# Kernel optimization log

Hardware: AMD Instinct MI355X
Metric: run time of the kernel (lower is better)

The kernel has to match this reference:

```python
import jax, jax.numpy as jnp
import numpy as np

N_HEADS = 8
KEY_DIM = 64
MEM_DIM = 64
HEAD_DIM = 64
IN_DIM = 256
OUT_DIM = 256


def setup_inputs() -> dict:
    key = jax.random.key(0)
    ks = jax.random.split(key, 7)
    x = jax.random.normal(ks[0], (8, IN_DIM, 64, 64), dtype=jnp.float32)
    # learned params
    key_p = jax.random.uniform(ks[1], (N_HEADS, KEY_DIM, MEM_DIM), dtype=jnp.float32)
    memory = jax.random.uniform(ks[2], (N_HEADS, MEM_DIM, HEAD_DIM), dtype=jnp.float32) * 0.5 - 0.25
    w_in = jax.random.normal(ks[3], (N_HEADS * KEY_DIM, IN_DIM), dtype=jnp.float32) * (1.0 / np.sqrt(IN_DIM))
    b_in = jax.random.normal(ks[4], (N_HEADS * KEY_DIM,), dtype=jnp.float32) * 0.01
    w_out = jax.random.normal(ks[5], (OUT_DIM, N_HEADS * HEAD_DIM), dtype=jnp.float32) * (1.0 / np.sqrt(N_HEADS * HEAD_DIM))
    b_out = jax.random.normal(ks[6], (OUT_DIM,), dtype=jnp.float32) * 0.01
    return {"x": x, "key_p": key_p, "memory": memory, "w_in": w_in, "b_in": b_in, "w_out": w_out, "b_out": b_out}


def reference(x, key_p, memory, w_in, b_in, w_out, b_out):
    B, _, H, W = x.shape
    # 1x1 conv projection: [B, n_heads*key_dim, H, W]
    out = jnp.einsum('oc,bchw->bohw', w_in, x) + b_in[None, :, None, None]
    # split heads: b (k n) h w -> b n k h w  (einops '(c m)' with m=n_heads => c is outer)
    out = out.reshape(B, KEY_DIM, N_HEADS, H, W).transpose(0, 2, 1, 3, 4)
    # per-head key matmul over key_dim -> memory_dim
    out = jnp.einsum('nkm,bnkhw->bnmhw', key_p, out)
    out = jax.nn.softmax(out, axis=2)
    # per-head memory matmul over memory_dim -> head_dim
    out = jnp.einsum('nmd,bnmhw->bndhw', memory, out)
    # merge heads: b n d h w -> b (d n) h w  (einops 'b m c h w -> b (m c) h w' with m=heads... wait)
    # einops 'b m c h w -> b (m c) h w': m (heads) is outer -> transpose then reshape
    out = out.reshape(B, N_HEADS * HEAD_DIM, H, W)
    # final 1x1 conv
    out = jnp.einsum('oc,bchw->bohw', w_out, out) + b_out[None, :, None, None]
    return out
```

## Files before the change

kernel.cpp:

```cpp
#include <hip/hip_runtime.h>


typedef _Float16 half8 __attribute__((ext_vector_type(8)));
typedef _Float16 half4 __attribute__((ext_vector_type(4)));
typedef _Float16 half2v __attribute__((ext_vector_type(2)));
typedef float float4v __attribute__((ext_vector_type(4)));

__device__ _Float16 g_Aswz[512 * 256];
__device__ _Float16 g_Mswz[256 * 512];
__device__ float    g_bb[512];

__global__ __launch_bounds__(256) void fold_all(
    const float* __restrict__ key_p, const float* __restrict__ w_in,
    const float* __restrict__ b_in, const float* __restrict__ w_out,
    const float* __restrict__ memory)
{
    __shared__ float sv[512];
    const int blk = blockIdx.x;
    const int t = threadIdx.x;

    if (blk < 512) {
        const int row = blk, n = row >> 6, m = row & 63;
        if (t < 64) sv[t] = key_p[n * 4096 + t * 64 + m];
        __syncthreads();
        const int c = t;
        float v = 0.f;
        #pragma unroll 8
        for (int k = 0; k < 64; ++k)
            v = fmaf(sv[k], w_in[(k * 8 + n) * 256 + c], v);
        int R = row >> 4, s = c >> 5, i = c & 7;
        int lidx = (row & 15) + 16 * ((c >> 3) & 3);
        g_Aswz[(((R * 8 + s) * 64 + lidx) << 3) + i] = (_Float16)v;
        if (t < 64) {
            float r2 = sv[t] * b_in[t * 8 + n];
            r2 += __shfl_down(r2, 32, 64);
            r2 += __shfl_down(r2, 16, 64);
            r2 += __shfl_down(r2, 8, 64);
            r2 += __shfl_down(r2, 4, 64);
            r2 += __shfl_down(r2, 2, 64);
            r2 += __shfl_down(r2, 1, 64);
            if (t == 0) g_bb[row] = r2;
        }
    } else {
        const int o = blk - 512;
        sv[t]       = w_out[o * 512 + t];
        sv[256 + t] = w_out[o * 512 + 256 + t];
        __syncthreads();
        #pragma unroll
        for (int hh = 0; hh < 2; ++hh) {
            int col = t + hh * 256, n = col >> 6, m = col & 63;
            const float4* mrow = (const float4*)(memory + n * 4096 + m * 64);
            const float4* wrow = (const float4*)(sv + n * 64);
            float v = 0.f;
            #pragma unroll
            for (int qd = 0; qd < 16; ++qd) {
                float4 a = mrow[qd], wv = wrow[qd];
                v += a.x * wv.x + a.y * wv.y + a.z * wv.z + a.w * wv.w;
            }
            int R2 = o >> 4, s = col >> 5, i = col & 7;
            int lidx = (o & 15) + 16 * ((col >> 3) & 3);
            g_Mswz[(((R2 * 16 + s) * 64 + lidx) << 3) + i] = (_Float16)v;
        }
    }
}

#define XS_STRIDE 264

__global__ __launch_bounds__(512) void fused_main(
    const float* __restrict__ x, const float* __restrict__ b_out,
    float* __restrict__ out)
{
    __shared__ _Float16 S[32768];

    const int t  = threadIdx.x;
    const int w  = t >> 6;
    const int l  = t & 63;
    const int q  = l >> 4;
    const int lp = l & 15;
    const int wg  = blockIdx.x;
    const int b   = wg >> 6;
    const int hw0 = (wg & 63) * 64;
    const float* xb = x + (size_t)b * 256 * 4096 + hw0;

    {
        const int m_ = t & 15;
        const int tc = t >> 4;
        #pragma unroll
        for (int i = 0; i < 4; ++i) {
            const int cp = i * 32 + tc;
            const int c0 = cp * 2;
            const float* p0 = xb + (size_t)c0 * 4096 + m_;
            const float* p1 = p0 + 4096;
            float a0 = p0[0],  a1 = p0[16], a2 = p0[32], a3 = p0[48];
            float b0 = p1[0],  b1 = p1[16], b2 = p1[32], b3 = p1[48];
            *(half2v*)(&S[(m_ +  0) * XS_STRIDE + c0]) = half2v{(_Float16)a0, (_Float16)b0};
            *(half2v*)(&S[(m_ + 16) * XS_STRIDE + c0]) = half2v{(_Float16)a1, (_Float16)b1};
            *(half2v*)(&S[(m_ + 32) * XS_STRIDE + c0]) = half2v{(_Float16)a2, (_Float16)b2};
            *(half2v*)(&S[(m_ + 48) * XS_STRIDE + c0]) = half2v{(_Float16)a3, (_Float16)b3};
        }
    }
    __syncthreads();

    float4v acc[4][4];
    #pragma unroll
    for (int r = 0; r < 4; ++r)
        #pragma unroll
        for (int c = 0; c < 4; ++c) acc[r][c] = float4v{0.f, 0.f, 0.f, 0.f};

    const half8* Ag = (const half8*)g_Aswz;
    for (int s = 0; s < 8; ++s) {
        half8 bf[4];
        #pragma unroll
        for (int c = 0; c < 4; ++c)
            bf[c] = *(const half8*)(&S[(c * 16 + lp) * XS_STRIDE + s * 32 + q * 8]);
        half8 af[4];
        #pragma unroll
        for (int r = 0; r < 4; ++r)
            af[r] = Ag[((w * 4 + r) * 8 + s) * 64 + l];
        #pragma unroll
        for (int r = 0; r < 4; ++r)
            #pragma unroll
            for (int c = 0; c < 4; ++c)
                acc[r][c] = __builtin_amdgcn_mfma_f32_16x16x32_f16(af[r], bf[c], acc[r][c], 0, 0, 0);
    }

    #pragma unroll
    for (int r = 0; r < 4; ++r) {
        float4v bbv = *(const float4v*)(g_bb + w * 64 + r * 16 + q * 4);
        #pragma unroll
        for (int c = 0; c < 4; ++c)
            #pragma unroll
            for (int j = 0; j < 4; ++j) acc[r][c][j] += bbv[j];
    }

    __syncthreads();

    #pragma unroll
    for (int c = 0; c < 4; ++c) {
        float mx = -1e30f;
        #pragma unroll
        for (int r = 0; r < 4; ++r)
            #pragma unroll
            for (int j = 0; j < 4; ++j) mx = fmaxf(mx, acc[r][c][j]);
        mx = fmaxf(mx, __shfl_xor(mx, 16, 64));
        mx = fmaxf(mx, __shfl_xor(mx, 32, 64));
        float sum = 0.f;
        #pragma unroll
        for (int r = 0; r < 4; ++r)
            #pragma unroll
            for (int j = 0; j < 4; ++j) {
                float e = __expf(acc[r][c][j] - mx);
                acc[r][c][j] = e;
                sum += e;
            }
        sum += __shfl_xor(sum, 16, 64);
        sum += __shfl_xor(sum, 32, 64);
        float inv = 1.f / sum;
        #pragma unroll
        for (int r = 0; r < 4; ++r) {
            int s2 = w * 2 + (r >> 1);
            int lq = ((r & 1) * 2 + (q >> 1)) * 16 + lp;
            int i0 = (q & 1) * 4;
            half4 pv = {(_Float16)(acc[r][c][0] * inv), (_Float16)(acc[r][c][1] * inv),
                        (_Float16)(acc[r][c][2] * inv), (_Float16)(acc[r][c][3] * inv)};
            *(half4*)(&S[(((s2 * 4 + c) * 64) + lq) * 8 + i0]) = pv;
        }
    }
    __syncthreads();

    float4v acc2[2][4];
    #pragma unroll
    for (int r = 0; r < 2; ++r)
        #pragma unroll
        for (int c = 0; c < 4; ++c) acc2[r][c] = float4v{0.f, 0.f, 0.f, 0.f};

    const half8* Mg = (const half8*)g_Mswz;
    for (int s2 = 0; s2 < 16; ++s2) {
        half8 bf2[4];
        #pragma unroll
        for (int c = 0; c < 4; ++c)
            bf2[c] = *(const half8*)(&S[(((s2 * 4 + c) * 64) + l) * 8]);
        half8 af2[2];
        #pragma unroll
        for (int r = 0; r < 2; ++r)
            af2[r] = Mg[((w * 2 + r) * 16 + s2) * 64 + l];
        #pragma unroll
        for (int r = 0; r < 2; ++r)
            #pragma unroll
            for (int c = 0; c < 4; ++c)
                acc2[r][c] = __builtin_amdgcn_mfma_f32_16x16x32_f16(af2[r], bf2[c], acc2[r][c], 0, 0, 0);
    }

    #pragma unroll
    for (int r = 0; r < 2; ++r) {
        int ob = w * 32 + r * 16 + q * 4;
        float4v bo = *(const float4v*)(b_out + ob);
        #pragma unroll
        for (int j = 0; j < 4; ++j) {
            float* orow = out + ((size_t)b * 256 + ob + j) * 4096 + hw0;
            #pragma unroll
            for (int c = 0; c < 4; ++c)
                orow[c * 16 + lp] = acc2[r][c][j] + bo[j];
        }
    }
}

extern "C" void kernel_launch(void* const* d_in, const int* in_sizes, int n_in,
                              void* d_out, int out_size, void* d_ws, size_t ws_size,
                              hipStream_t stream) {
    (void)in_sizes; (void)n_in; (void)ws_size; (void)out_size; (void)d_ws;
    const float* x      = (const float*)d_in[0];
    const float* key_p  = (const float*)d_in[1];
    const float* memory = (const float*)d_in[2];
    const float* w_in   = (const float*)d_in[3];
    const float* b_in   = (const float*)d_in[4];
    const float* w_out  = (const float*)d_in[5];
    const float* b_out  = (const float*)d_in[6];
    float* out = (float*)d_out;

    fold_all<<<768, 256, 0, stream>>>(key_p, w_in, b_in, w_out, memory);
    fused_main<<<512, 512, 0, stream>>>(x, b_out, out);
}
```

Measured before the change: 117.5 us.

## Process two pixel tiles per workgroup, prefetching the second tile into registers

Each workgroup now handles two 64-pixel tiles instead of one and launches 256 workgroups instead of 512. The second tile's x values are loaded into registers during the first tile's GEMM and then written to a separate LDS region, so the global load latency overlaps with compute. LDS grows to about 130KB and the softmax output gets its own region, which removes one barrier. The costs are fewer workgroups (256 on a GPU with 256 CUs, so one per CU), more register pressure, and no longer overlapping across workgroups.

```diff
diff --git a/kernel.cpp b/kernel.cpp
--- a/kernel.cpp
+++ b/kernel.cpp
@@ -65,38 +65,56 @@
 }
 
 #define XS_STRIDE 264
+#define XS1 16896
+#define PB  33792
 
 __global__ __launch_bounds__(512) void fused_main(
     const float* __restrict__ x, const float* __restrict__ b_out,
     float* __restrict__ out)
 {
-    __shared__ _Float16 S[32768];
+    __shared__ _Float16 S[66560];
 
     const int t  = threadIdx.x;
     const int w  = t >> 6;
     const int l  = t & 63;
     const int q  = l >> 4;
     const int lp = l & 15;
-    const int wg  = blockIdx.x;
-    const int b   = wg >> 6;
-    const int hw0 = (wg & 63) * 64;
-    const float* xb = x + (size_t)b * 256 * 4096 + hw0;
+    const int wg = blockIdx.x;
+    const int tile0 = wg * 2, tile1 = wg * 2 + 1;
+    const int b0 = tile0 >> 6, hw00 = (tile0 & 63) * 64;
+    const int b1 = tile1 >> 6, hw01 = (tile1 & 63) * 64;
+    const int m_ = t & 15;
+    const int tc = t >> 4;
+
+    const half8* Ag = (const half8*)g_Aswz;
+    const half8* Mg = (const half8*)g_Mswz;
 
     {
-        const int m_ = t & 15;
-        const int tc = t >> 4;
+        const float* xb = x + (size_t)b0 * 1048576 + hw00;
         #pragma unroll
         for (int i = 0; i < 4; ++i) {
-            const int cp = i * 32 + tc;
-            const int c0 = cp * 2;
+            const int c0 = (i * 32 + tc) * 2;
             const float* p0 = xb + (size_t)c0 * 4096 + m_;
             const float* p1 = p0 + 4096;
             float a0 = p0[0],  a1 = p0[16], a2 = p0[32], a3 = p0[48];
-            float b0 = p1[0],  b1 = p1[16], b2 = p1[32], b3 = p1[48];
-            *(half2v*)(&S[(m_ +  0) * XS_STRIDE + c0]) = half2v{(_Float16)a0, (_Float16)b0};
-            *(half2v*)(&S[(m_ + 16) * XS_STRIDE + c0]) = half2v{(_Float16)a1, (_Float16)b1};
-            *(half2v*)(&S[(m_ + 32) * XS_STRIDE + c0]) = half2v{(_Float16)a2, (_Float16)b2};
-            *(half2v*)(&S[(m_ + 48) * XS_STRIDE + c0]) = half2v{(_Float16)a3, (_Float16)b3};
+            float e0 = p1[0],  e1 = p1[16], e2 = p1[32], e3 = p1[48];
+            *(half2v*)(&S[(m_ +  0) * XS_STRIDE + c0]) = half2v{(_Float16)a0, (_Float16)e0};
+            *(half2v*)(&S[(m_ + 16) * XS_STRIDE + c0]) = half2v{(_Float16)a1, (_Float16)e1};
+            *(half2v*)(&S[(m_ + 32) * XS_STRIDE + c0]) = half2v{(_Float16)a2, (_Float16)e2};
+            *(half2v*)(&S[(m_ + 48) * XS_STRIDE + c0]) = half2v{(_Float16)a3, (_Float16)e3};
+        }
+    }
+
+    float h[4][8];
+    {
+        const float* xb = x + (size_t)b1 * 1048576 + hw01;
+        #pragma unroll
+        for (int i = 0; i < 4; ++i) {
+            const int c0 = (i * 32 + tc) * 2;
+            const float* p0 = xb + (size_t)c0 * 4096 + m_;
+            const float* p1 = p0 + 4096;
+            h[i][0] = p0[0];  h[i][1] = p0[16]; h[i][2] = p0[32]; h[i][3] = p0[48];
+            h[i][4] = p1[0];  h[i][5] = p1[16]; h[i][6] = p1[32]; h[i][7] = p1[48];
         }
     }
     __syncthreads();
@@ -107,7 +125,6 @@
         #pragma unroll
         for (int c = 0; c < 4; ++c) acc[r][c] = float4v{0.f, 0.f, 0.f, 0.f};
 
-    const half8* Ag = (const half8*)g_Aswz;
     for (int s = 0; s < 8; ++s) {
         half8 bf[4];
         #pragma unroll
@@ -125,6 +142,15 @@
     }
 
     #pragma unroll
+    for (int i = 0; i < 4; ++i) {
+        const int c0 = (i * 32 + tc) * 2;
+        *(half2v*)(&S[XS1 + (m_ +  0) * XS_STRIDE + c0]) = half2v{(_Float16)h[i][0], (_Float16)h[i][4]};
+        *(half2v*)(&S[XS1 + (m_ + 16) * XS_STRIDE + c0]) = half2v{(_Float16)h[i][1], (_Float16)h[i][5]};
+        *(half2v*)(&S[XS1 + (m_ + 32) * XS_STRIDE + c0]) = half2v{(_Float16)h[i][2], (_Float16)h[i][6]};
+        *(half2v*)(&S[XS1 + (m_ + 48) * XS_STRIDE + c0]) = half2v{(_Float16)h[i][3], (_Float16)h[i][7]};
+    }
+
+    #pragma unroll
     for (int r = 0; r < 4; ++r) {
         float4v bbv = *(const float4v*)(g_bb + w * 64 + r * 16 + q * 4);
         #pragma unroll
@@ -132,8 +158,6 @@
             #pragma unroll
             for (int j = 0; j < 4; ++j) acc[r][c][j] += bbv[j];
     }
-
-    __syncthreads();
 
     #pragma unroll
     for (int c = 0; c < 4; ++c) {
@@ -163,44 +187,144 @@
             int i0 = (q & 1) * 4;
             half4 pv = {(_Float16)(acc[r][c][0] * inv), (_Float16)(acc[r][c][1] * inv),
                         (_Float16)(acc[r][c][2] * inv), (_Float16)(acc[r][c][3] * inv)};
-            *(half4*)(&S[(((s2 * 4 + c) * 64) + lq) * 8 + i0]) = pv;
+            *(half4*)(&S[PB + (((s2 * 4 + c) * 64) + lq) * 8 + i0]) = pv;
         }
     }
     __syncthreads();
 
-    float4v acc2[2][4];
-    #pragma unroll
-    for (int r = 0; r < 2; ++r)
-        #pragma unroll
-        for (int c = 0; c < 4; ++c) acc2[r][c] = float4v{0.f, 0.f, 0.f, 0.f};
-
-    const half8* Mg = (const half8*)g_Mswz;
-    for (int s2 = 0; s2 < 16; ++s2) {
-        half8 bf2[4];
+    {
+        float4v acc2[2][4];
+        #pragma unroll
+        for (int r = 0; r < 2; ++r)
+            #pragma unroll
+            for (int c = 0; c < 4; ++c) acc2[r][c] = float4v{0.f, 0.f, 0.f, 0.f};
+
+        for (int s2 = 0; s2 < 16; ++s2) {
+            half8 bf2[4];
+            #pragma unroll
+            for (int c = 0; c < 4; ++c)
+                bf2[c] = *(const half8*)(&S[PB + (((s2 * 4 + c) * 64) + l) * 8]);
+            half8 af2[2];
+            #pragma unroll
+            for (int r = 0; r < 2; ++r)
+                af2[r] = Mg[((w * 2 + r) * 16 + s2) * 64 + l];
+            #pragma unroll
+            for (int r = 0; r < 2; ++r)
+                #pragma unroll
+                for (int c = 0; c < 4; ++c)
+                    acc2[r][c] = __builtin_amdgcn_mfma_f32_16x16x32_f16(af2[r], bf2[c], acc2[r][c], 0, 0, 0);
+        }
+        #pragma unroll
+        for (int r = 0; r < 2; ++r) {
+            int ob = w * 32 + r * 16 + q * 4;
+            float4v bo = *(const float4v*)(b_out + ob);
+            #pragma unroll
+            for (int j = 0; j < 4; ++j) {
+                float* orow = out + ((size_t)b0 * 256 + ob + j) * 4096 + hw00;
+                #pragma unroll
+                for (int c = 0; c < 4; ++c)
+                    orow[c * 16 + lp] = acc2[r][c][j] + bo[j];
+            }
+        }
+    }
+    __syncthreads();
+
+    #pragma unroll
+    for (int r = 0; r < 4; ++r)
+        #pragma unroll
+        for (int c = 0; c < 4; ++c) acc[r][c] = float4v{0.f, 0.f, 0.f, 0.f};
+
+    for (int s = 0; s < 8; ++s) {
+        half8 bf[4];
         #pragma unroll
         for (int c = 0; c < 4; ++c)
-            bf2[c] = *(const half8*)(&S[(((s2 * 4 + c) * 64) + l) * 8]);
-        half8 af2[2];
+            bf[c] = *(const half8*)(&S[XS1 + (c * 16 + lp) * XS_STRIDE + s * 32 + q * 8]);
+        half8 af[4];
+        #pragma unroll
+        for (int r = 0; r < 4; ++r)
+            af[r] = Ag[((w * 4 + r) * 8 + s) * 64 + l];
+        #pragma unroll
+        for (int r = 0; r < 4; ++r)
+            #pragma unroll
+            for (int c = 0; c < 4; ++c)
+                acc[r][c] = __builtin_amdgcn_mfma_f32_16x16x32_f16(af[r], bf[c], acc[r][c], 0, 0, 0);
+    }
+
+    #pragma unroll
+    for (int r = 0; r < 4; ++r) {
+        float4v bbv = *(const float4v*)(g_bb + w * 64 + r * 16 + q * 4);
+        #pragma unroll
+        for (int c = 0; c < 4; ++c)
+            #pragma unroll
+            for (int j = 0; j < 4; ++j) acc[r][c][j] += bbv[j];
+    }
+
+    #pragma unroll
+    for (int c = 0; c < 4; ++c) {
+        float mx = -1e30f;
+        #pragma unroll
+        for (int r = 0; r < 4; ++r)
+            #pragma unroll
+            for (int j = 0; j < 4; ++j) mx = fmaxf(mx, acc[r][c][j]);
+        mx = fmaxf(mx, __shfl_xor(mx, 16, 64));
+        mx = fmaxf(mx, __shfl_xor(mx, 32, 64));
+        float sum = 0.f;
+        #pragma unroll
+        for (int r = 0; r < 4; ++r)
+            #pragma unroll
+            for (int j = 0; j < 4; ++j) {
+                float e = __expf(acc[r][c][j] - mx);
+                acc[r][c][j] = e;
+                sum += e;
+            }
+        sum += __shfl_xor(sum, 16, 64);
+        sum += __shfl_xor(sum, 32, 64);
+        float inv = 1.f / sum;
+        #pragma unroll
+        for (int r = 0; r < 4; ++r) {
+            int s2 = w * 2 + (r >> 1);
+            int lq = ((r & 1) * 2 + (q >> 1)) * 16 + lp;
+            int i0 = (q & 1) * 4;
+            half4 pv = {(_Float16)(acc[r][c][0] * inv), (_Float16)(acc[r][c][1] * inv),
+                        (_Float16)(acc[r][c][2] * inv), (_Float16)(acc[r][c][3] * inv)};
+            *(half4*)(&S[PB + (((s2 * 4 + c) * 64) + lq) * 8 + i0]) = pv;
+        }
+    }
+    __syncthreads();
+
+    {
+        float4v acc2[2][4];
         #pragma unroll
         for (int r = 0; r < 2; ++r)
-            af2[r] = Mg[((w * 2 + r) * 16 + s2) * 64 + l];
-        #pragma unroll
-        for (int r = 0; r < 2; ++r)
+            #pragma unroll
+            for (int c = 0; c < 4; ++c) acc2[r][c] = float4v{0.f, 0.f, 0.f, 0.f};
+
+        for (int s2 = 0; s2 < 16; ++s2) {
+            half8 bf2[4];
             #pragma unroll
             for (int c = 0; c < 4; ++c)
-                acc2[r][c] = __builtin_amdgcn_mfma_f32_16x16x32_f16(af2[r], bf2[c], acc2[r][c], 0, 0, 0);
-    }
-
-    #pragma unroll
-    for (int r = 0; r < 2; ++r) {
-        int ob = w * 32 + r * 16 + q * 4;
-        float4v bo = *(const float4v*)(b_out + ob);
-        #pragma unroll
-        for (int j = 0; j < 4; ++j) {
-            float* orow = out + ((size_t)b * 256 + ob + j) * 4096 + hw0;
-            #pragma unroll
-            for (int c = 0; c < 4; ++c)
-                orow[c * 16 + lp] = acc2[r][c][j] + bo[j];
+                bf2[c] = *(const half8*)(&S[PB + (((s2 * 4 + c) * 64) + l) * 8]);
+            half8 af2[2];
+            #pragma unroll
+            for (int r = 0; r < 2; ++r)
+                af2[r] = Mg[((w * 2 + r) * 16 + s2) * 64 + l];
+            #pragma unroll
+            for (int r = 0; r < 2; ++r)
+                #pragma unroll
+                for (int c = 0; c < 4; ++c)
+                    acc2[r][c] = __builtin_amdgcn_mfma_f32_16x16x32_f16(af2[r], bf2[c], acc2[r][c], 0, 0, 0);
+        }
+        #pragma unroll
+        for (int r = 0; r < 2; ++r) {
+            int ob = w * 32 + r * 16 + q * 4;
+            float4v bo = *(const float4v*)(b_out + ob);
+            #pragma unroll
+            for (int j = 0; j < 4; ++j) {
+                float* orow = out + ((size_t)b1 * 256 + ob + j) * 4096 + hw01;
+                #pragma unroll
+                for (int c = 0; c < 4; ++c)
+                    orow[c * 16 + lp] = acc2[r][c][j] + bo[j];
+            }
         }
     }
 }
@@ -219,5 +343,5 @@
     float* out = (float*)d_out;
 
     fold_all<<<768, 256, 0, stream>>>(key_p, w_in, b_in, w_out, memory);
-    fused_main<<<512, 512, 0, stream>>>(x, b_out, out);
+    fused_main<<<256, 512, 0, stream>>>(x, b_out, out);
 }
```

Result: slower. 121.1 us (+3.1%).
